# Performance work log

Hardware: AMD Instinct MI355X
Metric: run time of the kernel (lower is better)

Reference implementation:

```python
import jax, jax.numpy as jnp
import numpy as np

B, L, DIM = 2, 1024, 1024
H, DH = 16, 64          # n_heads, dim_per_head
GS = 1                  # group_size
T = 3 * GS              # triplet heads (last T heads, head_choice==0)
HN = H - T              # normal heads
DG = DH * GS            # triplet 'pseudo-head' dim
SCALE = 1.0 / np.sqrt(DH)


def setup_inputs() -> dict:
    key = jax.random.key(0)
    ks = jax.random.split(key, 12)
    s = 0.02
    return {
        'query': jax.random.normal(ks[0], (B, L, DIM), jnp.float32),
        'key':   jax.random.normal(ks[1], (B, L, DIM), jnp.float32),
        'value': jax.random.normal(ks[2], (B, L, DIM), jnp.float32),
        'mask':  jnp.ones((B, L), dtype=jnp.int32),
        'Wq': jax.random.normal(ks[3], (DIM, DIM), jnp.float32) * s,
        'bq': jnp.zeros((DIM,), jnp.float32),
        'Wk': jax.random.normal(ks[4], (DIM, DIM), jnp.float32) * s,
        'bk': jnp.zeros((DIM,), jnp.float32),
        'Wv': jax.random.normal(ks[5], (DIM, DIM), jnp.float32) * s,
        'bv': jnp.zeros((DIM,), jnp.float32),
        'Wo': jax.random.normal(ks[6], (DIM, DIM), jnp.float32) * s,
        'bo': jnp.zeros((DIM,), jnp.float32),
    }


def _split_heads(x, W, b):
    # x: [B,L,DIM] -> [B,H,L,DH]
    return (x @ W.T + b).reshape(B, L, H, DH).transpose(0, 2, 1, 3)


def _triplet_reshape(x):
    # [B,T,L,DH] -> [B,L,T,DH] -> [B,L,DG,3] -> [B,DG,L,3]
    return x.transpose(0, 2, 1, 3).reshape(B, L, DG, 3).transpose(0, 2, 1, 3)


def reference(query, key, value, mask, Wq, bq, Wk, bk, Wv, bv, Wo, bo):
    q = _split_heads(query, Wq, bq)
    k = _split_heads(key, Wk, bk)
    v = _split_heads(value, Wv, bv)

    # head split: last T heads go to the triplet branch (head_choice == 0)
    qn, qt = q[:, :HN], q[:, HN:]
    kn, kt = k[:, :HN], k[:, HN:]
    vn, vt = v[:, :HN], v[:, HN:]

    # ---- triplet branch (layer in Tlayers) ----
    qtr = _triplet_reshape(qt)   # [B,DG,L,3]
    ktr = _triplet_reshape(kt)
    vtr = _triplet_reshape(vt)

    # key2_flag==1: key_triplet2 = clone; permute_type=[2] => roll index by 1 along L
    idx = jnp.roll(jnp.arange(L), 1)
    kt2 = ktr[:, :, idx, :]
    K_cross = jnp.cross(ktr, kt2, axis=-1)                 # [B,DG,L,3]

    attn_t = jnp.einsum('bdlt,bdmt->bdlm', qtr, K_cross)   # [B,DG,L,L]
    # permute_back==0, random_flag==0: inverse permutation along last dim
    inv = jnp.argsort(idx)
    attn_t = attn_t[..., inv]
    # absolute_flag==1
    attn_t = jnp.abs(attn_t)

    # ---- normal attention ----
    scores = jnp.einsum('bhld,bhmd->bhlm', qn * SCALE, kn)  # [B,HN,L,L]
    pad = (mask == 0)[:, None, None, :]
    scores = jnp.where(pad, -jnp.inf, scores)
    w = jax.nn.softmax(scores, axis=-1)                     # dropout p=0

    wt = jax.nn.softmax(attn_t * SCALE, axis=-1)            # [B,DG,L,L]

    ctx = jnp.einsum('bhlm,bhmd->bhld', w, vn)              # [B,HN,L,DH]
    ctx = ctx.transpose(0, 2, 1, 3).reshape(B, L, HN * DH)

    ctx_t = jnp.einsum('bdlm,bdmt->bdlt', wt, vtr)          # [B,DG,L,3]
    ctx_t = ctx_t.transpose(0, 2, 1, 3).reshape(B, L, DG * 3)

    context = jnp.concatenate([ctx, ctx_t], axis=-1)        # [B,L,DIM]
    return context @ Wo.T + bo
```

## Files before the change

kernel.cpp:

```cpp
#include <hip/hip_runtime.h>

#define L_SEQ 1024
typedef unsigned short ush;
typedef __attribute__((ext_vector_type(8))) short short8;
typedef __attribute__((ext_vector_type(4))) float f32x4;

#define MFMA __builtin_amdgcn_mfma_f32_16x16x32_bf16

#define Q_PRESCALE 0.18033688011112042f

__device__ __forceinline__ ush f2bf(float x) {
  union { float f; unsigned u; } c; c.f = x;
  unsigned r = c.u + 0x7FFF + ((c.u >> 16) & 1);
  return (ush)(r >> 16);
}
__device__ __forceinline__ float bf2f(ush h) {
  union { unsigned u; float f; } c; c.u = ((unsigned)h) << 16;
  return c.f;
}
__device__ __forceinline__ void gload16(const void* g, void* l) {
  __builtin_amdgcn_global_load_lds(
      (const __attribute__((address_space(1))) unsigned*)g,
      (__attribute__((address_space(3))) unsigned*)l, 16, 0, 0);
}

struct SplitA {
  const float* s0; const float* s1; const float* s2; const float* s3;
  const float* s4; const float* s5; const float* s6;
  ush* d0; ush* d1; ush* d2; ush* d3; ush* d4; ush* d5; ush* d6;
};
__global__ __launch_bounds__(256) void split_all(SplitA a) {
  const int ti = blockIdx.y;
  const float* s; ush* d; int n;
  switch (ti) {
    case 0: s = a.s0; d = a.d0; n = 1 << 21; break;
    case 1: s = a.s1; d = a.d1; n = 1 << 21; break;
    case 2: s = a.s2; d = a.d2; n = 1 << 21; break;
    case 3: s = a.s3; d = a.d3; n = 1 << 20; break;
    case 4: s = a.s4; d = a.d4; n = 1 << 20; break;
    case 5: s = a.s5; d = a.d5; n = 1 << 20; break;
    default: s = a.s6; d = a.d6; n = 1 << 20; break;
  }
  int i = (blockIdx.x * 256 + threadIdx.x) * 8;
  if (i >= n) return;
  float4 x0 = *(const float4*)(s + i);
  float4 x1 = *(const float4*)(s + i + 4);
  float xs[8] = {x0.x, x0.y, x0.z, x0.w, x1.x, x1.y, x1.z, x1.w};
  ush h[8], l[8];
  #pragma unroll
  for (int j = 0; j < 8; j++) {
    h[j] = f2bf(xs[j]);
    l[j] = f2bf(xs[j] - bf2f(h[j]));
  }
  ushort4 h0 = {h[0], h[1], h[2], h[3]}, h1 = {h[4], h[5], h[6], h[7]};
  ushort4 l0 = {l[0], l[1], l[2], l[3]}, l1 = {l[4], l[5], l[6], l[7]};
  *(ushort4*)(d + i) = h0;     *(ushort4*)(d + i + 4) = h1;
  *(ushort4*)(d + n + i) = l0; *(ushort4*)(d + n + i + 4) = l1;
}

__global__ __launch_bounds__(256) void gemm_sp(
    const ush* __restrict__ Abase, long AzStride, long Aplane,
    const ush* __restrict__ Bbase, long BzStride,
    const float* __restrict__ b0, const float* __restrict__ b1,
    const float* __restrict__ b2,
    float* __restrict__ Yf, ush* __restrict__ Pbase) {
  __shared__ __align__(16) ush lds[24576];
  const int t = threadIdx.x;
  const int z = blockIdx.z;
  const ush* A = Abase + (size_t)z * AzStride;
  const ush* B = Bbase + (size_t)z * BzStride;
  const float* bias = (z == 0) ? b0 : (z == 1) ? b1 : b2;
  const long Bplane = 1024 * 1024;
  const int r0 = blockIdx.x * 128;
  const int n0 = blockIdx.y * 64;
  const int wid = t >> 6, lane = t & 63;
  const int wr = wid >> 1, wc = wid & 1;
  const int sr = t >> 3, ss = t & 7;
  const int sd = ss ^ (sr & 7);
  const int fr = lane & 15, fk = lane >> 4;

  f32x4 acc[4][2];
  #pragma unroll
  for (int mf = 0; mf < 4; mf++)
    #pragma unroll
    for (int nf = 0; nf < 2; nf++)
      acc[mf][nf] = (f32x4){0.f, 0.f, 0.f, 0.f};

  const ush* Ag = A + (size_t)(r0 + sr) * 1024 + sd * 8;
  const ush* Bg = B + (size_t)(n0 + sr) * 1024 + sd * 8;

  for (int k0 = 0; k0 < 1024; k0 += 64) {
    __syncthreads();
    #pragma unroll
    for (int p = 0; p < 2; p++)
      #pragma unroll
      for (int c = 0; c < 4; c++)
        gload16(Ag + (size_t)p * Aplane + (size_t)c * 32 * 1024 + k0,
                lds + p * 8192 + (c * 256 + t) * 8);
    #pragma unroll
    for (int p = 0; p < 2; p++)
      #pragma unroll
      for (int c = 0; c < 2; c++)
        gload16(Bg + (size_t)p * Bplane + (size_t)c * 32 * 1024 + k0,
                lds + 16384 + p * 4096 + (c * 256 + t) * 8);
    __syncthreads();
    #pragma unroll
    for (int g = 0; g < 2; g++) {
      short8 ah[4], al[4], bh[2], bl[2];
      const int sl = ((g * 4 + fk) ^ (fr & 7)) * 8;
      #pragma unroll
      for (int mf = 0; mf < 4; mf++) {
        int row = wr * 64 + mf * 16 + fr;
        ah[mf] = *(const short8*)(lds + row * 64 + sl);
        al[mf] = *(const short8*)(lds + 8192 + row * 64 + sl);
      }
      #pragma unroll
      for (int nf = 0; nf < 2; nf++) {
        int row = wc * 32 + nf * 16 + fr;
        bh[nf] = *(const short8*)(lds + 16384 + row * 64 + sl);
        bl[nf] = *(const short8*)(lds + 20480 + row * 64 + sl);
      }
      #pragma unroll
      for (int mf = 0; mf < 4; mf++)
        #pragma unroll
        for (int nf = 0; nf < 2; nf++) {
          acc[mf][nf] = MFMA(ah[mf], bh[nf], acc[mf][nf], 0, 0, 0);
          acc[mf][nf] = MFMA(ah[mf], bl[nf], acc[mf][nf], 0, 0, 0);
          acc[mf][nf] = MFMA(al[mf], bh[nf], acc[mf][nf], 0, 0, 0);
        }
    }
  }
  const float oscale = (z == 0) ? Q_PRESCALE : 1.0f;
  ush* Ph = Pbase ? (Pbase + (size_t)z * 4194304) : (ush*)0;
  ush* Pl = Ph ? Ph + 2097152 : (ush*)0;
  #pragma unroll
  for (int nf = 0; nf < 2; nf++) {
    const int col = n0 + wc * 32 + nf * 16 + fr;
    const float bb = bias[col];
    #pragma unroll
    for (int mf = 0; mf < 4; mf++) {
      const int rowb = r0 + wr * 64 + mf * 16 + fk * 4;
      if (Yf) {
        #pragma unroll
        for (int r = 0; r < 4; r++)
          Yf[(size_t)(rowb + r) * 1024 + col] = acc[mf][nf][r] + bb;
      } else if (z != 2) {
        #pragma unroll
        for (int r = 0; r < 4; r++) {
          float v = (acc[mf][nf][r] + bb) * oscale;
          ush hv = f2bf(v);
          Ph[(size_t)(rowb + r) * 1024 + col] = hv;
          Pl[(size_t)(rowb + r) * 1024 + col] = f2bf(v - bf2f(hv));
        }
      } else {
        ushort4 hv, lv;
        #pragma unroll
        for (int r = 0; r < 4; r++) {
          float v = acc[mf][nf][r] + bb;
          ush h = f2bf(v);
          ((ush*)&hv)[r] = h;
          ((ush*)&lv)[r] = f2bf(v - bf2f(h));
        }
        *(ushort4*)&Ph[(size_t)col * 2048 + rowb] = hv;
        *(ushort4*)&Pl[(size_t)col * 2048 + rowb] = lv;
      }
    }
  }
}

__global__ __launch_bounds__(256) void attn_norm(
    const ush* __restrict__ qh, const ush* __restrict__ ql,
    const ush* __restrict__ kh, const ush* __restrict__ kl,
    const ush* __restrict__ vth,
    ush* __restrict__ ctxh, ush* __restrict__ ctxl) {
  __shared__ __align__(16) ush Qh[4096], Ql[4096];
  __shared__ __align__(16) ush Kh[2][4096], Kl[2][4096], Vt[2][4096];
  __shared__ __align__(16) ush Pb[64 * 72];
  const int t = threadIdx.x;
  const int b = blockIdx.z, h = blockIdx.y;
  const int l0 = blockIdx.x * 64;
  const int hoff = h * 64;
  const int lane = t & 63, w = t >> 6;
  const int c = lane & 15, g = lane >> 4;
  const int srow = t >> 3, sg = t & 7;

  #pragma unroll
  for (int cc = 0; cc < 2; cc++) {
    int row = cc * 32 + srow;
    int slot = sg ^ (row & 7);
    size_t src = (size_t)(b * 1024 + l0 + row) * 1024 + hoff + slot * 8;
    gload16(qh + src, Qh + row * 64 + sg * 8);
    gload16(ql + src, Ql + row * 64 + sg * 8);
  }
  auto stageKV = [&](int buf, int m0) {
    #pragma unroll
    for (int cc = 0; cc < 2; cc++) {
      int row = cc * 32 + srow;
      int slot = sg ^ (row & 7);
      size_t srck = (size_t)(b * 1024 + m0 + row) * 1024 + hoff + slot * 8;
      gload16(kh + srck, &Kh[buf][row * 64 + sg * 8]);
      gload16(kl + srck, &Kl[buf][row * 64 + sg * 8]);
      size_t srcv = (size_t)(hoff + row) * 2048 + b * 1024 + m0 + slot * 8;
      gload16(vth + srcv, &Vt[buf][row * 64 + sg * 8]);
    }
  };
  stageKV(0, 0);
  __syncthreads();

  short8 ah[2], al[2];
  #pragma unroll
  for (int kk = 0; kk < 2; kk++) {
    int q = w * 16 + c;
    int slot = (kk * 4 + g) ^ (q & 7);
    ah[kk] = *(const short8*)(Qh + q * 64 + slot * 8);
    al[kk] = *(const short8*)(Ql + q * 64 + slot * 8);
  }
  const short8 ones = {0x3F80, 0x3F80, 0x3F80, 0x3F80,
                       0x3F80, 0x3F80, 0x3F80, 0x3F80};

  f32x4 acc[4];
  f32x4 accD = {0.f, 0.f, 0.f, 0.f};
  #pragma unroll
  for (int df = 0; df < 4; df++) acc[df] = (f32x4){0.f, 0.f, 0.f, 0.f};

  for (int step = 0; step < 16; step++) {
    const int cur = step & 1;
    if (step < 15) stageKV(cur ^ 1, (step + 1) * 64);
    const ush* KhC = &Kh[cur][0];
    const ush* KlC = &Kl[cur][0];
    const ush* VtC = &Vt[cur][0];
    f32x4 s[4];
    #pragma unroll
    for (int nf = 0; nf < 4; nf++) {
      s[nf] = (f32x4){0.f, 0.f, 0.f, 0.f};
      #pragma unroll
      for (int kk = 0; kk < 2; kk++) {
        int kr = nf * 16 + c;
        int slot = (kk * 4 + g) ^ (kr & 7);
        short8 bh = *(const short8*)(KhC + kr * 64 + slot * 8);
        short8 bl = *(const short8*)(KlC + kr * 64 + slot * 8);
        s[nf] = MFMA(ah[kk], bh, s[nf], 0, 0, 0);
        s[nf] = MFMA(ah[kk], bl, s[nf], 0, 0, 0);
        s[nf] = MFMA(al[kk], bh, s[nf], 0, 0, 0);
      }
    }
    #pragma unroll
    for (int nf = 0; nf < 4; nf++) {
      float p0 = exp2f(s[nf][0]), p1 = exp2f(s[nf][1]);
      float p2 = exp2f(s[nf][2]), p3 = exp2f(s[nf][3]);
      unsigned u01, u23;
      asm("v_cvt_pk_bf16_f32 %0, %1, %2" : "=v"(u01) : "v"(p0), "v"(p1));
      asm("v_cvt_pk_bf16_f32 %0, %1, %2" : "=v"(u23) : "v"(p2), "v"(p3));
      ush* base = Pb + (w * 16 + g * 4) * 72 + nf * 16 + c;
      base[0 * 72] = (ush)u01;
      base[1 * 72] = (ush)(u01 >> 16);
      base[2 * 72] = (ush)u23;
      base[3 * 72] = (ush)(u23 >> 16);
    }
    #pragma unroll
    for (int kk = 0; kk < 2; kk++) {
      short8 pa = *(const short8*)(Pb + (w * 16 + c) * 72 + (kk * 4 + g) * 8);
      accD = MFMA(pa, ones, accD, 0, 0, 0);
      #pragma unroll
      for (int df = 0; df < 4; df++) {
        int dr = df * 16 + c;
        int slot = (kk * 4 + g) ^ (dr & 7);
        short8 bv = *(const short8*)(VtC + dr * 64 + slot * 8);
        acc[df] = MFMA(pa, bv, acc[df], 0, 0, 0);
      }
    }
    __syncthreads();
  }
  float inv[4];
  #pragma unroll
  for (int r = 0; r < 4; r++) inv[r] = 1.0f / accD[r];
  #pragma unroll
  for (int df = 0; df < 4; df++)
    #pragma unroll
    for (int r = 0; r < 4; r++) {
      float o = acc[df][r] * inv[r];
      size_t off = (size_t)(b * 1024 + l0 + w * 16 + g * 4 + r) * 1024 + hoff + df * 16 + c;
      ush hv = f2bf(o);
      ctxh[off] = hv;
      ctxl[off] = f2bf(o - bf2f(hv));
    }
}

__global__ __launch_bounds__(256) void trip_kc(
    const ush* __restrict__ kh, const ush* __restrict__ kl,
    ush* __restrict__ kc4g) {
  const int t = threadIdx.x;
  const int m = blockIdx.x * 256 + t;
  const int d = blockIdx.y, b = blockIdx.z;
  const int col = 832 + 3 * d;
  size_t r0 = (size_t)(b * 1024 + m) * 1024 + col;
  size_t r1 = (size_t)(b * 1024 + ((m + 1) & 1023)) * 1024 + col;
  float c0 = bf2f(kh[r0]) + bf2f(kl[r0]);
  float c1 = bf2f(kh[r0 + 1]) + bf2f(kl[r0 + 1]);
  float c2 = bf2f(kh[r0 + 2]) + bf2f(kl[r0 + 2]);
  float a0 = bf2f(kh[r1]) + bf2f(kl[r1]);
  float a1 = bf2f(kh[r1 + 1]) + bf2f(kl[r1 + 1]);
  float a2 = bf2f(kh[r1 + 2]) + bf2f(kl[r1 + 2]);
  ushort4 o;
  o.x = f2bf(a1 * c2 - a2 * c1);
  o.y = f2bf(a2 * c0 - a0 * c2);
  o.z = f2bf(a0 * c1 - a1 * c0);
  o.w = 0;
  *(ushort4*)(kc4g + ((size_t)(b * 64 + d) * 1024 + m) * 4) = o;
}

__global__ __launch_bounds__(256) void attn_trip_mfma(
    const ush* __restrict__ kc4g,
    const ush* __restrict__ qh, const ush* __restrict__ ql,
    const ush* __restrict__ vth,
    ush* __restrict__ ctxh, ush* __restrict__ ctxl) {
  __shared__ __align__(16) ush KC[4096];
  __shared__ __align__(16) ush VT[4 * 1040];
  __shared__ __align__(16) ush PB[4][16][36];
  const int t = threadIdx.x;
  const int l0 = blockIdx.x * 64;
  const int d = blockIdx.y, b = blockIdx.z;
  const int col = 832 + 3 * d;
  const int lane = t & 63, w = t >> 6;
  const int c = lane & 15, g = lane >> 4;

  const ush* kcsrc = kc4g + (size_t)(b * 64 + d) * 4096;
  gload16(kcsrc + t * 8, KC + t * 8);
  gload16(kcsrc + 2048 + t * 8, KC + 2048 + t * 8);

  {
    int row = t >> 6, chunk = t & 63;
    ush* dst = VT + row * 1040 + chunk * 16;
    if (row < 3) {
      const ush* src = vth + (size_t)(col + row) * 2048 + b * 1024 + chunk * 16;
      uint4 v0 = *(const uint4*)(src);
      uint4 v1 = *(const uint4*)(src + 8);
      *(uint4*)(dst) = v0;
      *(uint4*)(dst + 8) = v1;
    } else {
      uint4 ones = {0x3F803F80u, 0x3F803F80u, 0x3F803F80u, 0x3F803F80u};
      *(uint4*)(dst) = ones;
      *(uint4*)(dst + 8) = ones;
    }
  }

  short8 qB = {0, 0, 0, 0, 0, 0, 0, 0};
  {
    size_t qr = (size_t)(b * 1024 + l0 + w * 16 + c) * 1024 + col;
    float q0 = bf2f(qh[qr]) + bf2f(ql[qr]);
    float q1 = bf2f(qh[qr + 1]) + bf2f(ql[qr + 1]);
    float q2 = bf2f(qh[qr + 2]) + bf2f(ql[qr + 2]);
    if (g == 0) {
      qB[0] = (short)f2bf(q0);
      qB[1] = (short)f2bf(q1);
      qB[2] = (short)f2bf(q2);
    }
  }
  __syncthreads();

  f32x4 acc = {0.f, 0.f, 0.f, 0.f};
  ush* pb = &PB[w][0][0];
  #pragma unroll 2
  for (int m0 = 0; m0 < 1024; m0 += 32) {
    short8 a0 = {0, 0, 0, 0, 0, 0, 0, 0}, a1 = {0, 0, 0, 0, 0, 0, 0, 0};
    *(uint2*)&a0 = *(const uint2*)(KC + (m0 + c) * 4);
    *(uint2*)&a1 = *(const uint2*)(KC + (m0 + 16 + c) * 4);
    f32x4 z = {0.f, 0.f, 0.f, 0.f};
    f32x4 s0 = MFMA(a0, qB, z, 0, 0, 0);
    f32x4 s1 = MFMA(a1, qB, z, 0, 0, 0);
    float p0 = exp2f(fabsf(s0[0])), p1 = exp2f(fabsf(s0[1]));
    float p2 = exp2f(fabsf(s0[2])), p3 = exp2f(fabsf(s0[3]));
    float p4 = exp2f(fabsf(s1[0])), p5 = exp2f(fabsf(s1[1]));
    float p6 = exp2f(fabsf(s1[2])), p7 = exp2f(fabsf(s1[3]));
    unsigned k01, k23, k45, k67;
    asm("v_cvt_pk_bf16_f32 %0, %1, %2" : "=v"(k01) : "v"(p0), "v"(p1));
    asm("v_cvt_pk_bf16_f32 %0, %1, %2" : "=v"(k23) : "v"(p2), "v"(p3));
    asm("v_cvt_pk_bf16_f32 %0, %1, %2" : "=v"(k45) : "v"(p4), "v"(p5));
    asm("v_cvt_pk_bf16_f32 %0, %1, %2" : "=v"(k67) : "v"(p6), "v"(p7));
    *(uint2*)(pb + c * 36 + 4 * g) = (uint2){k01, k23};
    *(uint2*)(pb + c * 36 + 16 + 4 * g) = (uint2){k45, k67};
    short8 pf;
    *(uint2*)&pf = *(const uint2*)(pb + c * 36 + 8 * g);
    *((uint2*)&pf + 1) = *(const uint2*)(pb + c * 36 + 8 * g + 4);
    short8 vf = *(const short8*)(VT + (c & 3) * 1040 + m0 + 8 * g);
    acc = MFMA(vf, pf, acc, 0, 0, 0);
  }
  if (g == 0) {
    const float inv = 1.0f / acc[3];
    size_t off = (size_t)(b * 1024 + l0 + w * 16 + c) * 1024 + col;
    #pragma unroll
    for (int comp = 0; comp < 3; comp++) {
      float o = acc[comp] * inv;
      ush hv = f2bf(o);
      ctxh[off + comp] = hv;
      ctxl[off + comp] = f2bf(o - bf2f(hv));
    }
  }
}

extern "C" void kernel_launch(void* const* d_in, const int* in_sizes, int n_in,
                              void* d_out, int out_size, void* d_ws, size_t ws_size,
                              hipStream_t stream) {
  const float* query = (const float*)d_in[0];
  const float* key   = (const float*)d_in[1];
  const float* value = (const float*)d_in[2];
  const float* Wq = (const float*)d_in[4];
  const float* bq = (const float*)d_in[5];
  const float* Wk = (const float*)d_in[6];
  const float* bk = (const float*)d_in[7];
  const float* Wv = (const float*)d_in[8];
  const float* bv = (const float*)d_in[9];
  const float* Wo = (const float*)d_in[10];
  const float* bo = (const float*)d_in[11];
  float* out = (float*)d_out;

  char* W = (char*)d_ws;
  const size_t MB = 1 << 20;
  ush* qs  = (ush*)(W + 0 * MB);
  ush* ks  = (ush*)(W + 8 * MB);
  ush* vs  = (ush*)(W + 16 * MB);
  ush* Wqs = (ush*)(W + 24 * MB);
  ush* Wks = (ush*)(W + 28 * MB);
  ush* Wvs = (ush*)(W + 32 * MB);
  ush* Wos = (ush*)(W + 36 * MB);
  ush* planes = (ush*)(W + 40 * MB);
  ush* qh  = planes;
  ush* ql  = planes + 2097152;
  ush* khp = planes + 4194304;
  ush* klp = planes + 6291456;
  ush* vth = planes + 8388608;
  ush* ctxh = qs;
  ush* ctxl = qs + 2097152;
  ush* kc4g = ks;

  SplitA sa = {query, key, value, Wq, Wk, Wv, Wo,
               qs, ks, vs, Wqs, Wks, Wvs, Wos};
  split_all<<<dim3(1024, 7), 256, 0, stream>>>(sa);

  gemm_sp<<<dim3(16, 16, 3), 256, 0, stream>>>(
      qs, (long)(4 * 1024 * 1024), (long)(2 * 1024 * 1024),
      Wqs, (long)(2 * 1024 * 1024),
      bq, bk, bv,
      (float*)0, planes);

  trip_kc<<<dim3(4, 64, 2), 256, 0, stream>>>(khp, klp, kc4g);

  attn_norm<<<dim3(16, 13, 2), 256, 0, stream>>>(qh, ql, khp, klp, vth, ctxh, ctxl);
  attn_trip_mfma<<<dim3(16, 64, 2), 256, 0, stream>>>(kc4g, qh, ql, vth, ctxh, ctxl);

  gemm_sp<<<dim3(16, 16, 1), 256, 0, stream>>>(
      ctxh, 0L, (long)(2 * 1024 * 1024),
      Wos, 0L,
      bo, bo, bo,
      out, (ush*)0);
}
```

Baseline: 172.2 us.

## Fuse normal and triplet attention into one launch, double-buffer output GEMM

Merges the normal-head and triplet attention kernels into a single launch that dispatches on block index and shares LDS through a union. This removes one launch and lets the two kinds of blocks run concurrently, filling the machine better. It also adds a templated double-buffered K loop to the output projection GEMM, drops the low-precision V plane write, and reorganizes the P staging in normal attention. The V split drop lowers accuracy slightly, and the double buffer doubles LDS use, which may reduce occupancy.

```diff
diff --git a/kernel.cpp b/kernel.cpp
--- a/kernel.cpp
+++ b/kernel.cpp
@@ -58,13 +58,14 @@
   *(ushort4*)(d + n + i) = l0; *(ushort4*)(d + n + i + 4) = l1;
 }
 
+template <int DBUF>
 __global__ __launch_bounds__(256) void gemm_sp(
     const ush* __restrict__ Abase, long AzStride, long Aplane,
     const ush* __restrict__ Bbase, long BzStride,
     const float* __restrict__ b0, const float* __restrict__ b1,
     const float* __restrict__ b2,
     float* __restrict__ Yf, ush* __restrict__ Pbase) {
-  __shared__ __align__(16) ush lds[24576];
+  __shared__ __align__(16) ush lds[DBUF ? 49152 : 24576];
   const int t = threadIdx.x;
   const int z = blockIdx.z;
   const ush* A = Abase + (size_t)z * AzStride;
@@ -89,21 +90,21 @@
   const ush* Ag = A + (size_t)(r0 + sr) * 1024 + sd * 8;
   const ush* Bg = B + (size_t)(n0 + sr) * 1024 + sd * 8;
 
-  for (int k0 = 0; k0 < 1024; k0 += 64) {
-    __syncthreads();
+  auto stage = [&](ush* Lb, int k0) {
     #pragma unroll
     for (int p = 0; p < 2; p++)
       #pragma unroll
       for (int c = 0; c < 4; c++)
         gload16(Ag + (size_t)p * Aplane + (size_t)c * 32 * 1024 + k0,
-                lds + p * 8192 + (c * 256 + t) * 8);
+                Lb + p * 8192 + (c * 256 + t) * 8);
     #pragma unroll
     for (int p = 0; p < 2; p++)
       #pragma unroll
       for (int c = 0; c < 2; c++)
         gload16(Bg + (size_t)p * Bplane + (size_t)c * 32 * 1024 + k0,
-                lds + 16384 + p * 4096 + (c * 256 + t) * 8);
-    __syncthreads();
+                Lb + 16384 + p * 4096 + (c * 256 + t) * 8);
+  };
+  auto compute = [&](const ush* Lb) {
     #pragma unroll
     for (int g = 0; g < 2; g++) {
       short8 ah[4], al[4], bh[2], bl[2];
@@ -111,14 +112,14 @@
       #pragma unroll
       for (int mf = 0; mf < 4; mf++) {
         int row = wr * 64 + mf * 16 + fr;
-        ah[mf] = *(const short8*)(lds + row * 64 + sl);
-        al[mf] = *(const short8*)(lds + 8192 + row * 64 + sl);
+        ah[mf] = *(const short8*)(Lb + row * 64 + sl);
+        al[mf] = *(const short8*)(Lb + 8192 + row * 64 + sl);
       }
       #pragma unroll
       for (int nf = 0; nf < 2; nf++) {
         int row = wc * 32 + nf * 16 + fr;
-        bh[nf] = *(const short8*)(lds + 16384 + row * 64 + sl);
-        bl[nf] = *(const short8*)(lds + 20480 + row * 64 + sl);
+        bh[nf] = *(const short8*)(Lb + 16384 + row * 64 + sl);
+        bl[nf] = *(const short8*)(Lb + 20480 + row * 64 + sl);
       }
       #pragma unroll
       for (int mf = 0; mf < 4; mf++)
@@ -129,7 +130,26 @@
           acc[mf][nf] = MFMA(al[mf], bh[nf], acc[mf][nf], 0, 0, 0);
         }
     }
+  };
+
+  if constexpr (DBUF) {
+    stage(lds, 0);
+    __syncthreads();
+    for (int k0 = 0; k0 < 1024; k0 += 64) {
+      const int cur = (k0 >> 6) & 1;
+      if (k0 + 64 < 1024) stage(lds + (cur ^ 1) * 24576, k0 + 64);
+      compute(lds + cur * 24576);
+      __syncthreads();
+    }
+  } else {
+    for (int k0 = 0; k0 < 1024; k0 += 64) {
+      __syncthreads();
+      stage(lds, k0);
+      __syncthreads();
+      compute(lds);
+    }
   }
+
   const float oscale = (z == 0) ? Q_PRESCALE : 1.0f;
   ush* Ph = Pbase ? (Pbase + (size_t)z * 4194304) : (ush*)0;
   ush* Pl = Ph ? Ph + 2097152 : (ush*)0;
@@ -153,137 +173,14 @@
           Pl[(size_t)(rowb + r) * 1024 + col] = f2bf(v - bf2f(hv));
         }
       } else {
-        ushort4 hv, lv;
-        #pragma unroll
-        for (int r = 0; r < 4; r++) {
-          float v = acc[mf][nf][r] + bb;
-          ush h = f2bf(v);
-          ((ush*)&hv)[r] = h;
-          ((ush*)&lv)[r] = f2bf(v - bf2f(h));
-        }
+        ushort4 hv;
+        #pragma unroll
+        for (int r = 0; r < 4; r++)
+          ((ush*)&hv)[r] = f2bf(acc[mf][nf][r] + bb);
         *(ushort4*)&Ph[(size_t)col * 2048 + rowb] = hv;
-        *(ushort4*)&Pl[(size_t)col * 2048 + rowb] = lv;
       }
     }
   }
-}
-
-__global__ __launch_bounds__(256) void attn_norm(
-    const ush* __restrict__ qh, const ush* __restrict__ ql,
-    const ush* __restrict__ kh, const ush* __restrict__ kl,
-    const ush* __restrict__ vth,
-    ush* __restrict__ ctxh, ush* __restrict__ ctxl) {
-  __shared__ __align__(16) ush Qh[4096], Ql[4096];
-  __shared__ __align__(16) ush Kh[2][4096], Kl[2][4096], Vt[2][4096];
-  __shared__ __align__(16) ush Pb[64 * 72];
-  const int t = threadIdx.x;
-  const int b = blockIdx.z, h = blockIdx.y;
-  const int l0 = blockIdx.x * 64;
-  const int hoff = h * 64;
-  const int lane = t & 63, w = t >> 6;
-  const int c = lane & 15, g = lane >> 4;
-  const int srow = t >> 3, sg = t & 7;
-
-  #pragma unroll
-  for (int cc = 0; cc < 2; cc++) {
-    int row = cc * 32 + srow;
-    int slot = sg ^ (row & 7);
-    size_t src = (size_t)(b * 1024 + l0 + row) * 1024 + hoff + slot * 8;
-    gload16(qh + src, Qh + row * 64 + sg * 8);
-    gload16(ql + src, Ql + row * 64 + sg * 8);
-  }
-  auto stageKV = [&](int buf, int m0) {
-    #pragma unroll
-    for (int cc = 0; cc < 2; cc++) {
-      int row = cc * 32 + srow;
-      int slot = sg ^ (row & 7);
-      size_t srck = (size_t)(b * 1024 + m0 + row) * 1024 + hoff + slot * 8;
-      gload16(kh + srck, &Kh[buf][row * 64 + sg * 8]);
-      gload16(kl + srck, &Kl[buf][row * 64 + sg * 8]);
-      size_t srcv = (size_t)(hoff + row) * 2048 + b * 1024 + m0 + slot * 8;
-      gload16(vth + srcv, &Vt[buf][row * 64 + sg * 8]);
-    }
-  };
-  stageKV(0, 0);
-  __syncthreads();
-
-  short8 ah[2], al[2];
-  #pragma unroll
-  for (int kk = 0; kk < 2; kk++) {
-    int q = w * 16 + c;
-    int slot = (kk * 4 + g) ^ (q & 7);
-    ah[kk] = *(const short8*)(Qh + q * 64 + slot * 8);
-    al[kk] = *(const short8*)(Ql + q * 64 + slot * 8);
-  }
-  const short8 ones = {0x3F80, 0x3F80, 0x3F80, 0x3F80,
-                       0x3F80, 0x3F80, 0x3F80, 0x3F80};
-
-  f32x4 acc[4];
-  f32x4 accD = {0.f, 0.f, 0.f, 0.f};
-  #pragma unroll
-  for (int df = 0; df < 4; df++) acc[df] = (f32x4){0.f, 0.f, 0.f, 0.f};
-
-  for (int step = 0; step < 16; step++) {
-    const int cur = step & 1;
-    if (step < 15) stageKV(cur ^ 1, (step + 1) * 64);
-    const ush* KhC = &Kh[cur][0];
-    const ush* KlC = &Kl[cur][0];
-    const ush* VtC = &Vt[cur][0];
-    f32x4 s[4];
-    #pragma unroll
-    for (int nf = 0; nf < 4; nf++) {
-      s[nf] = (f32x4){0.f, 0.f, 0.f, 0.f};
-      #pragma unroll
-      for (int kk = 0; kk < 2; kk++) {
-        int kr = nf * 16 + c;
-        int slot = (kk * 4 + g) ^ (kr & 7);
-        short8 bh = *(const short8*)(KhC + kr * 64 + slot * 8);
-        short8 bl = *(const short8*)(KlC + kr * 64 + slot * 8);
-        s[nf] = MFMA(ah[kk], bh, s[nf], 0, 0, 0);
-        s[nf] = MFMA(ah[kk], bl, s[nf], 0, 0, 0);
-        s[nf] = MFMA(al[kk], bh, s[nf], 0, 0, 0);
-      }
-    }
-    #pragma unroll
-    for (int nf = 0; nf < 4; nf++) {
-      float p0 = exp2f(s[nf][0]), p1 = exp2f(s[nf][1]);
-      float p2 = exp2f(s[nf][2]), p3 = exp2f(s[nf][3]);
-      unsigned u01, u23;
-      asm("v_cvt_pk_bf16_f32 %0, %1, %2" : "=v"(u01) : "v"(p0), "v"(p1));
-      asm("v_cvt_pk_bf16_f32 %0, %1, %2" : "=v"(u23) : "v"(p2), "v"(p3));
-      ush* base = Pb + (w * 16 + g * 4) * 72 + nf * 16 + c;
-      base[0 * 72] = (ush)u01;
-      base[1 * 72] = (ush)(u01 >> 16);
-      base[2 * 72] = (ush)u23;
-      base[3 * 72] = (ush)(u23 >> 16);
-    }
-    #pragma unroll
-    for (int kk = 0; kk < 2; kk++) {
-      short8 pa = *(const short8*)(Pb + (w * 16 + c) * 72 + (kk * 4 + g) * 8);
-      accD = MFMA(pa, ones, accD, 0, 0, 0);
-      #pragma unroll
-      for (int df = 0; df < 4; df++) {
-        int dr = df * 16 + c;
-        int slot = (kk * 4 + g) ^ (dr & 7);
-        short8 bv = *(const short8*)(VtC + dr * 64 + slot * 8);
-        acc[df] = MFMA(pa, bv, acc[df], 0, 0, 0);
-      }
-    }
-    __syncthreads();
-  }
-  float inv[4];
-  #pragma unroll
-  for (int r = 0; r < 4; r++) inv[r] = 1.0f / accD[r];
-  #pragma unroll
-  for (int df = 0; df < 4; df++)
-    #pragma unroll
-    for (int r = 0; r < 4; r++) {
-      float o = acc[df][r] * inv[r];
-      size_t off = (size_t)(b * 1024 + l0 + w * 16 + g * 4 + r) * 1024 + hoff + df * 16 + c;
-      ush hv = f2bf(o);
-      ctxh[off] = hv;
-      ctxl[off] = f2bf(o - bf2f(hv));
-    }
 }
 
 __global__ __launch_bounds__(256) void trip_kc(
@@ -309,91 +206,215 @@
   *(ushort4*)(kc4g + ((size_t)(b * 64 + d) * 1024 + m) * 4) = o;
 }
 
-__global__ __launch_bounds__(256) void attn_trip_mfma(
-    const ush* __restrict__ kc4g,
+struct NormLds {
+  ush Kh[2][4096];
+  ush Kl[2][4096];
+  ush Vt[2][4096];
+  unsigned Pb[4][16][20];
+};
+struct TripLds {
+  ush KC[4096];
+  ush VT[4 * 1040];
+  ush PB[4][16][36];
+};
+union FusedLds { NormLds n; TripLds t; };
+
+__global__ __launch_bounds__(256) void attn_fused(
     const ush* __restrict__ qh, const ush* __restrict__ ql,
-    const ush* __restrict__ vth,
+    const ush* __restrict__ kh, const ush* __restrict__ kl,
+    const ush* __restrict__ vth, const ush* __restrict__ kc4g,
     ush* __restrict__ ctxh, ush* __restrict__ ctxl) {
-  __shared__ __align__(16) ush KC[4096];
-  __shared__ __align__(16) ush VT[4 * 1040];
-  __shared__ __align__(16) ush PB[4][16][36];
+  __shared__ __align__(16) FusedLds L;
   const int t = threadIdx.x;
-  const int l0 = blockIdx.x * 64;
-  const int d = blockIdx.y, b = blockIdx.z;
-  const int col = 832 + 3 * d;
+  const int bid = blockIdx.x;
   const int lane = t & 63, w = t >> 6;
   const int c = lane & 15, g = lane >> 4;
 
-  const ush* kcsrc = kc4g + (size_t)(b * 64 + d) * 4096;
-  gload16(kcsrc + t * 8, KC + t * 8);
-  gload16(kcsrc + 2048 + t * 8, KC + 2048 + t * 8);
-
-  {
-    int row = t >> 6, chunk = t & 63;
-    ush* dst = VT + row * 1040 + chunk * 16;
-    if (row < 3) {
-      const ush* src = vth + (size_t)(col + row) * 2048 + b * 1024 + chunk * 16;
-      uint4 v0 = *(const uint4*)(src);
-      uint4 v1 = *(const uint4*)(src + 8);
-      *(uint4*)(dst) = v0;
-      *(uint4*)(dst + 8) = v1;
-    } else {
-      uint4 ones = {0x3F803F80u, 0x3F803F80u, 0x3F803F80u, 0x3F803F80u};
-      *(uint4*)(dst) = ones;
-      *(uint4*)(dst + 8) = ones;
-    }
-  }
-
-  short8 qB = {0, 0, 0, 0, 0, 0, 0, 0};
-  {
-    size_t qr = (size_t)(b * 1024 + l0 + w * 16 + c) * 1024 + col;
-    float q0 = bf2f(qh[qr]) + bf2f(ql[qr]);
-    float q1 = bf2f(qh[qr + 1]) + bf2f(ql[qr + 1]);
-    float q2 = bf2f(qh[qr + 2]) + bf2f(ql[qr + 2]);
+  if (bid < 416) {
+    const int l0 = (bid & 15) * 64;
+    const int rem = bid >> 4;
+    const int h = rem % 13, b = rem / 13;
+    const int hoff = h * 64;
+    const int srow = t >> 3, sg = t & 7;
+
+    #pragma unroll
+    for (int cc = 0; cc < 2; cc++) {
+      int row = cc * 32 + srow;
+      int slot = sg ^ (row & 7);
+      size_t src = (size_t)(b * 1024 + l0 + row) * 1024 + hoff + slot * 8;
+      gload16(qh + src, &L.n.Kh[1][row * 64 + sg * 8]);
+      gload16(ql + src, &L.n.Kl[1][row * 64 + sg * 8]);
+    }
+    auto stageKV = [&](int buf, int m0) {
+      #pragma unroll
+      for (int cc = 0; cc < 2; cc++) {
+        int row = cc * 32 + srow;
+        int slot = sg ^ (row & 7);
+        size_t srck = (size_t)(b * 1024 + m0 + row) * 1024 + hoff + slot * 8;
+        gload16(kh + srck, &L.n.Kh[buf][row * 64 + sg * 8]);
+        gload16(kl + srck, &L.n.Kl[buf][row * 64 + sg * 8]);
+        size_t srcv = (size_t)(hoff + row) * 2048 + b * 1024 + m0 + slot * 8;
+        gload16(vth + srcv, &L.n.Vt[buf][row * 64 + sg * 8]);
+      }
+    };
+    stageKV(0, 0);
+    __syncthreads();
+
+    short8 ah[2], al[2];
+    #pragma unroll
+    for (int kk = 0; kk < 2; kk++) {
+      int q = w * 16 + c;
+      int slot = (kk * 4 + g) ^ (q & 7);
+      ah[kk] = *(const short8*)(&L.n.Kh[1][q * 64 + slot * 8]);
+      al[kk] = *(const short8*)(&L.n.Kl[1][q * 64 + slot * 8]);
+    }
+    __syncthreads();
+
+    const short8 ones = {0x3F80, 0x3F80, 0x3F80, 0x3F80,
+                         0x3F80, 0x3F80, 0x3F80, 0x3F80};
+    f32x4 acc[4];
+    f32x4 accD = {0.f, 0.f, 0.f, 0.f};
+    #pragma unroll
+    for (int df = 0; df < 4; df++) acc[df] = (f32x4){0.f, 0.f, 0.f, 0.f};
+
+    for (int step = 0; step < 16; step++) {
+      const int cur = step & 1;
+      if (step < 15) stageKV(cur ^ 1, (step + 1) * 64);
+      const ush* KhC = &L.n.Kh[cur][0];
+      const ush* KlC = &L.n.Kl[cur][0];
+      const ush* VtC = &L.n.Vt[cur][0];
+      f32x4 s[4];
+      #pragma unroll
+      for (int nf = 0; nf < 4; nf++) {
+        s[nf] = (f32x4){0.f, 0.f, 0.f, 0.f};
+        #pragma unroll
+        for (int kk = 0; kk < 2; kk++) {
+          int kr = nf * 16 + c;
+          int slot = (kk * 4 + g) ^ (kr & 7);
+          short8 bh = *(const short8*)(KhC + kr * 64 + slot * 8);
+          short8 bl = *(const short8*)(KlC + kr * 64 + slot * 8);
+          s[nf] = MFMA(bh, ah[kk], s[nf], 0, 0, 0);
+          s[nf] = MFMA(bh, al[kk], s[nf], 0, 0, 0);
+          s[nf] = MFMA(bl, ah[kk], s[nf], 0, 0, 0);
+        }
+      }
+      float pr[4][4];
+      #pragma unroll
+      for (int nf = 0; nf < 4; nf++)
+        #pragma unroll
+        for (int r = 0; r < 4; r++) pr[nf][r] = exp2f(s[nf][r]);
+      #pragma unroll
+      for (int kk = 0; kk < 2; kk++) {
+        #pragma unroll
+        for (int nn = 0; nn < 2; nn++) {
+          const int nf = kk * 2 + nn;
+          unsigned u0, u1;
+          asm("v_cvt_pk_bf16_f32 %0, %1, %2" : "=v"(u0) : "v"(pr[nf][0]), "v"(pr[nf][1]));
+          asm("v_cvt_pk_bf16_f32 %0, %1, %2" : "=v"(u1) : "v"(pr[nf][2]), "v"(pr[nf][3]));
+          *(uint2*)&L.n.Pb[w][c][nn * 8 + g * 2] = (uint2){u0, u1};
+        }
+        short8 pa = *(const short8*)&L.n.Pb[w][c][g * 4];
+        accD = MFMA(pa, ones, accD, 0, 0, 0);
+        #pragma unroll
+        for (int df = 0; df < 4; df++) {
+          int dr = df * 16 + c;
+          int slot = (kk * 4 + g) ^ (dr & 7);
+          short8 bv = *(const short8*)(VtC + dr * 64 + slot * 8);
+          acc[df] = MFMA(pa, bv, acc[df], 0, 0, 0);
+        }
+      }
+      __syncthreads();
+    }
+    float inv[4];
+    #pragma unroll
+    for (int r = 0; r < 4; r++) inv[r] = 1.0f / accD[r];
+    #pragma unroll
+    for (int df = 0; df < 4; df++)
+      #pragma unroll
+      for (int r = 0; r < 4; r++) {
+        float o = acc[df][r] * inv[r];
+        size_t off = (size_t)(b * 1024 + l0 + w * 16 + g * 4 + r) * 1024 + hoff + df * 16 + c;
+        ush hv = f2bf(o);
+        ctxh[off] = hv;
+        ctxl[off] = f2bf(o - bf2f(hv));
+      }
+  } else {
+    const int t2 = bid - 416;
+    const int l0 = (t2 & 15) * 64;
+    const int d = (t2 >> 4) & 63, b = t2 >> 10;
+    const int col = 832 + 3 * d;
+
+    const ush* kcsrc = kc4g + (size_t)(b * 64 + d) * 4096;
+    gload16(kcsrc + t * 8, L.t.KC + t * 8);
+    gload16(kcsrc + 2048 + t * 8, L.t.KC + 2048 + t * 8);
+
+    {
+      int row = t >> 6, chunk = t & 63;
+      ush* dst = L.t.VT + row * 1040 + chunk * 16;
+      if (row < 3) {
+        const ush* src = vth + (size_t)(col + row) * 2048 + b * 1024 + chunk * 16;
+        uint4 v0 = *(const uint4*)(src);
+        uint4 v1 = *(const uint4*)(src + 8);
+        *(uint4*)(dst) = v0;
+        *(uint4*)(dst + 8) = v1;
+      } else {
+        uint4 onesv = {0x3F803F80u, 0x3F803F80u, 0x3F803F80u, 0x3F803F80u};
+        *(uint4*)(dst) = onesv;
+        *(uint4*)(dst + 8) = onesv;
+      }
+    }
+
+    short8 qB = {0, 0, 0, 0, 0, 0, 0, 0};
+    {
+      size_t qr = (size_t)(b * 1024 + l0 + w * 16 + c) * 1024 + col;
+      float q0 = bf2f(qh[qr]) + bf2f(ql[qr]);
+      float q1 = bf2f(qh[qr + 1]) + bf2f(ql[qr + 1]);
+      float q2 = bf2f(qh[qr + 2]) + bf2f(ql[qr + 2]);
+      if (g == 0) {
+        qB[0] = (short)f2bf(q0);
+        qB[1] = (short)f2bf(q1);
+        qB[2] = (short)f2bf(q2);
+      }
+    }
+    __syncthreads();
+
+    f32x4 acc = {0.f, 0.f, 0.f, 0.f};
+    ush* pb = &L.t.PB[w][0][0];
+    #pragma unroll 2
+    for (int m0 = 0; m0 < 1024; m0 += 32) {
+      short8 a0 = {0, 0, 0, 0, 0, 0, 0, 0}, a1 = {0, 0, 0, 0, 0, 0, 0, 0};
+      *(uint2*)&a0 = *(const uint2*)(L.t.KC + (m0 + c) * 4);
+      *(uint2*)&a1 = *(const uint2*)(L.t.KC + (m0 + 16 + c) * 4);
+      f32x4 z = {0.f, 0.f, 0.f, 0.f};
+      f32x4 s0 = MFMA(a0, qB, z, 0, 0, 0);
+      f32x4 s1 = MFMA(a1, qB, z, 0, 0, 0);
+      float p0 = exp2f(fabsf(s0[0])), p1 = exp2f(fabsf(s0[1]));
+      float p2 = exp2f(fabsf(s0[2])), p3 = exp2f(fabsf(s0[3]));
+      float p4 = exp2f(fabsf(s1[0])), p5 = exp2f(fabsf(s1[1]));
+      float p6 = exp2f(fabsf(s1[2])), p7 = exp2f(fabsf(s1[3]));
+      unsigned k01, k23, k45, k67;
+      asm("v_cvt_pk_bf16_f32 %0, %1, %2" : "=v"(k01) : "v"(p0), "v"(p1));
+      asm("v_cvt_pk_bf16_f32 %0, %1, %2" : "=v"(k23) : "v"(p2), "v"(p3));
+      asm("v_cvt_pk_bf16_f32 %0, %1, %2" : "=v"(k45) : "v"(p4), "v"(p5));
+      asm("v_cvt_pk_bf16_f32 %0, %1, %2" : "=v"(k67) : "v"(p6), "v"(p7));
+      *(uint2*)(pb + c * 36 + 4 * g) = (uint2){k01, k23};
+      *(uint2*)(pb + c * 36 + 16 + 4 * g) = (uint2){k45, k67};
+      short8 pf;
+      *(uint2*)&pf = *(const uint2*)(pb + c * 36 + 8 * g);
+      *((uint2*)&pf + 1) = *(const uint2*)(pb + c * 36 + 8 * g + 4);
+      short8 vf = *(const short8*)(L.t.VT + (c & 3) * 1040 + m0 + 8 * g);
+      acc = MFMA(vf, pf, acc, 0, 0, 0);
+    }
     if (g == 0) {
-      qB[0] = (short)f2bf(q0);
-      qB[1] = (short)f2bf(q1);
-      qB[2] = (short)f2bf(q2);
-    }
-  }
-  __syncthreads();
-
-  f32x4 acc = {0.f, 0.f, 0.f, 0.f};
-  ush* pb = &PB[w][0][0];
-  #pragma unroll 2
-  for (int m0 = 0; m0 < 1024; m0 += 32) {
-    short8 a0 = {0, 0, 0, 0, 0, 0, 0, 0}, a1 = {0, 0, 0, 0, 0, 0, 0, 0};
-    *(uint2*)&a0 = *(const uint2*)(KC + (m0 + c) * 4);
-    *(uint2*)&a1 = *(const uint2*)(KC + (m0 + 16 + c) * 4);
-    f32x4 z = {0.f, 0.f, 0.f, 0.f};
-    f32x4 s0 = MFMA(a0, qB, z, 0, 0, 0);
-    f32x4 s1 = MFMA(a1, qB, z, 0, 0, 0);
-    float p0 = exp2f(fabsf(s0[0])), p1 = exp2f(fabsf(s0[1]));
-    float p2 = exp2f(fabsf(s0[2])), p3 = exp2f(fabsf(s0[3]));
-    float p4 = exp2f(fabsf(s1[0])), p5 = exp2f(fabsf(s1[1]));
-    float p6 = exp2f(fabsf(s1[2])), p7 = exp2f(fabsf(s1[3]));
-    unsigned k01, k23, k45, k67;
-    asm("v_cvt_pk_bf16_f32 %0, %1, %2" : "=v"(k01) : "v"(p0), "v"(p1));
-    asm("v_cvt_pk_bf16_f32 %0, %1, %2" : "=v"(k23) : "v"(p2), "v"(p3));
-    asm("v_cvt_pk_bf16_f32 %0, %1, %2" : "=v"(k45) : "v"(p4), "v"(p5));
-    asm("v_cvt_pk_bf16_f32 %0, %1, %2" : "=v"(k67) : "v"(p6), "v"(p7));
-    *(uint2*)(pb + c * 36 + 4 * g) = (uint2){k01, k23};
-    *(uint2*)(pb + c * 36 + 16 + 4 * g) = (uint2){k45, k67};
-    short8 pf;
-    *(uint2*)&pf = *(const uint2*)(pb + c * 36 + 8 * g);
-    *((uint2*)&pf + 1) = *(const uint2*)(pb + c * 36 + 8 * g + 4);
-    short8 vf = *(const short8*)(VT + (c & 3) * 1040 + m0 + 8 * g);
-    acc = MFMA(vf, pf, acc, 0, 0, 0);
-  }
-  if (g == 0) {
-    const float inv = 1.0f / acc[3];
-    size_t off = (size_t)(b * 1024 + l0 + w * 16 + c) * 1024 + col;
-    #pragma unroll
-    for (int comp = 0; comp < 3; comp++) {
-      float o = acc[comp] * inv;
-      ush hv = f2bf(o);
-      ctxh[off + comp] = hv;
-      ctxl[off + comp] = f2bf(o - bf2f(hv));
+      const float inv = 1.0f / acc[3];
+      size_t off = (size_t)(b * 1024 + l0 + w * 16 + c) * 1024 + col;
+      #pragma unroll
+      for (int comp = 0; comp < 3; comp++) {
+        float o = acc[comp] * inv;
+        ush hv = f2bf(o);
+        ctxh[off + comp] = hv;
+        ctxl[off + comp] = f2bf(o - bf2f(hv));
+      }
     }
   }
 }
@@ -437,7 +458,7 @@
                qs, ks, vs, Wqs, Wks, Wvs, Wos};
   split_all<<<dim3(1024, 7), 256, 0, stream>>>(sa);
 
-  gemm_sp<<<dim3(16, 16, 3), 256, 0, stream>>>(
+  gemm_sp<0><<<dim3(16, 16, 3), 256, 0, stream>>>(
       qs, (long)(4 * 1024 * 1024), (long)(2 * 1024 * 1024),
       Wqs, (long)(2 * 1024 * 1024),
       bq, bk, bv,
@@ -445,10 +466,10 @@
 
   trip_kc<<<dim3(4, 64, 2), 256, 0, stream>>>(khp, klp, kc4g);
 
-  attn_norm<<<dim3(16, 13, 2), 256, 0, stream>>>(qh, ql, khp, klp, vth, ctxh, ctxl);
-  attn_trip_mfma<<<dim3(16, 64, 2), 256, 0, stream>>>(kc4g, qh, ql, vth, ctxh, ctxl);
-
-  gemm_sp<<<dim3(16, 16, 1), 256, 0, stream>>>(
+  attn_fused<<<dim3(416 + 2048), 256, 0, stream>>>(
+      qh, ql, khp, klp, vth, kc4g, ctxh, ctxl);
+
+  gemm_sp<1><<<dim3(16, 16, 1), 256, 0, stream>>>(
       ctxh, 0L, (long)(2 * 1024 * 1024),
       Wos, 0L,
       bo, bo, bo,
```

New measurement: 158.6 us. 1.09x faster.
